# Performance work log

Measured on AMD Instinct MI355X. Metric: run time of the kernel, lower is better.

## Reference

```python
import jax, jax.numpy as jnp
import numpy as np

SR = 16000
N_TAPS = 10
MIN_F = 50.0
MAX_F = 2000.0


def setup_inputs() -> dict:
    key = jax.random.key(0)
    k1, k2 = jax.random.split(key)
    x = jax.random.normal(k1, (8, 1, 32000), dtype=jnp.float32)
    # raw f params as in the module: 3*(rand*2-1) in [-3, 3]
    f = 3.0 * (jax.random.uniform(k2, (128, 1), dtype=jnp.float32) * 2.0 - 1.0)
    a = jnp.full((128, 1), 0.9, dtype=jnp.float32)
    return {"x": x, "f": f, "a": a}


def _comb(x, f_raw, a):
    # scaling_function (min_freq/max_freq branch, no bins):
    # f = min_freq * (max_freq/min_freq) ** sigmoid(f_raw)
    fratio = MAX_F / MIN_F
    f = MIN_F * fratio ** jax.nn.sigmoid(f_raw)  # [O, I] fundamental freq in Hz

    B, I, T = x.shape
    O = f.shape[0]
    D = SR / f  # [O, I] fractional delay in samples (one period)
    n = jnp.arange(T, dtype=x.dtype)
    ci = jnp.arange(I)[None, :, None]  # channel index for gather, [1, I, 1]

    acc = jnp.zeros((B, O, T), dtype=x.dtype)
    # y[b,o,t] = sum_i sum_{k=0}^{n_taps-1} a[o,i]^k * lerp(x[b,i, t - k*D[o,i]])
    for k in range(N_TAPS):
        pos = n[None, None, :] - k * D[:, :, None]  # [O, I, T] fractional read positions
        i0 = jnp.floor(pos)
        frac = (pos - i0).astype(x.dtype)
        valid = (i0 >= 0).astype(x.dtype)  # causal: zero before signal start
        i0i = jnp.clip(i0.astype(jnp.int32), 0, T - 1)
        i1i = jnp.clip(i0i + 1, 0, T - 1)
        x0 = x[:, ci, i0i]  # [B, O, I, T]
        x1 = x[:, ci, i1i]  # [B, O, I, T]
        tap = (x0 * (1.0 - frac) + x1 * frac) * valid
        acc = acc + jnp.sum((a ** k)[None, :, :, None] * tap, axis=2)
    return acc


def reference(x, f, a):
    # use_bias=False -> b = 0, gain g unused in forward
    return _comb(x, f, a)
```

## Files before the change

### kernel.cpp

```cpp
#include <hip/hip_runtime.h>
#include <math.h>

#define T_LEN 32000
#define B_N 8
#define O_N 128
#define NTAPS 10
#define TILE_T 1280
#define NT 5
#define PAD 2944
#define NSTAGE (TILE_T + PAD + 1)
#define NSTAGE_AL ((NSTAGE + 3) & ~3)
#define OCHUNK 8
#define TC 640

__global__ __launch_bounds__(128) void comb_params_kernel(
    const float* __restrict__ f, const float* __restrict__ a,
    float* __restrict__ tp) {
  int o = threadIdx.x;
  double fr = (double)f[o];
  double sig = 1.0 / (1.0 + exp(-fr));
  float ff = (float)(50.0 * pow(40.0, sig));
  float D = 16000.0f / ff;
  float av = a[o];
  for (int k = 0; k < NTAPS; ++k) {
    tp[o * 20 + k] = (float)k * D;
    tp[o * 20 + 10 + k] = (float)pow((double)av, (double)k);
  }
}

__device__ __forceinline__ void comb_body_fast(const float* __restrict__ tp,
                                               float* __restrict__ outp,
                                               const float* sx, int oc,
                                               int t0, int tid) {
  float tcf = (float)(t0 + TC);
  int cbase = PAD - t0 - TC;
  float xt[NT];
#pragma unroll
  for (int j = 0; j < NT; ++j) xt[j] = sx[PAD + tid + 256 * j];
#pragma unroll 1
  for (int oi = 0; oi < OCHUNK; ++oi) {
    const float4* p4 = (const float4*)(tp + (oc + oi) * 20);
    float4 q0 = p4[0], q1 = p4[1], q2 = p4[2], q3 = p4[3], q4 = p4[4];
    float kD[NTAPS] = {q0.x, q0.y, q0.z, q0.w, q1.x, q1.y, q1.z, q1.w, q2.x, q2.y};
    float ak[NTAPS] = {q2.z, q2.w, q3.x, q3.y, q3.z, q3.w, q4.x, q4.y, q4.z, q4.w};
    float acc[NT];
#pragma unroll
    for (int j = 0; j < NT; ++j) acc[j] = xt[j];
#pragma unroll
    for (int k = 1; k < NTAPS; ++k) {
      float pc = tcf - kD[k];
      float fc = __builtin_amdgcn_fractf(pc);
      int sb = (int)(pc - fc) + cbase + tid;
      float w1 = ak[k] * fc;
      float w0 = ak[k] - w1;
#pragma unroll
      for (int j = 0; j < NT; ++j) {
        int idx = sb + 256 * j;
        float x0 = sx[idx];
        float x1 = sx[idx + 1];
        acc[j] = fmaf(w0, x0, fmaf(w1, x1, acc[j]));
      }
    }
#pragma unroll
    for (int j = 0; j < NT; ++j)
      outp[(size_t)oi * T_LEN + 256 * j] = acc[j];
  }
}

__device__ __forceinline__ void comb_body_edge(const float* __restrict__ tp,
                                               float* __restrict__ outp,
                                               const float* sx, int oc,
                                               const float* tf, int base_g) {
#pragma unroll 1
  for (int oi = 0; oi < OCHUNK; ++oi) {
    const float4* p4 = (const float4*)(tp + (oc + oi) * 20);
    float4 q0 = p4[0], q1 = p4[1], q2 = p4[2], q3 = p4[3], q4 = p4[4];
    float kD[NTAPS] = {q0.x, q0.y, q0.z, q0.w, q1.x, q1.y, q1.z, q1.w, q2.x, q2.y};
    float ak[NTAPS] = {q2.z, q2.w, q3.x, q3.y, q3.z, q3.w, q4.x, q4.y, q4.z, q4.w};
    float acc[NT];
#pragma unroll
    for (int j = 0; j < NT; ++j) acc[j] = 0.0f;
#pragma unroll
    for (int k = 0; k < NTAPS; ++k) {
#pragma unroll
      for (int j = 0; j < NT; ++j) {
        float pos = tf[j] - kD[k];
        float frac = __builtin_amdgcn_fractf(pos);
        int idx = (int)pos - base_g;
        float x0 = sx[idx];
        float x1 = sx[idx + 1];
        float tap = fmaf(frac, x1 - x0, x0);
        tap = (pos >= 0.0f) ? tap : 0.0f;
        acc[j] = fmaf(ak[k], tap, acc[j]);
      }
    }
#pragma unroll
    for (int j = 0; j < NT; ++j)
      outp[(size_t)oi * T_LEN + 256 * j] = acc[j];
  }
}

__global__ __launch_bounds__(256) void comb_main_kernel(
    const float* __restrict__ x, const float* __restrict__ tp,
    float* __restrict__ out) {
  __shared__ float sx[NSTAGE_AL];
  int bx = blockIdx.x;
  int t0 = bx * TILE_T;
  int b = blockIdx.y;
  int oc = blockIdx.z * OCHUNK;
  const float* __restrict__ xrow = x + b * T_LEN;
  int base_g = t0 - PAD;
  int tid = threadIdx.x;

  if (bx >= 3 && bx <= 23) {
    float4* s4 = (float4*)sx;
    const float4* g4 = (const float4*)(xrow + base_g);
#pragma unroll 1
    for (int j = tid; j < NSTAGE_AL / 4; j += 256) s4[j] = g4[j];
  } else {
#pragma unroll 1
    for (int j = tid; j < NSTAGE_AL; j += 256) {
      int g = base_g + j;
      float v = 0.0f;
      if (g >= 0) v = xrow[g < T_LEN - 1 ? g : T_LEN - 1];
      sx[j] = v;
    }
  }
  __syncthreads();

  float* outp = out + ((size_t)b * O_N + oc) * T_LEN + t0 + tid;

  if (bx >= 3) {
    comb_body_fast(tp, outp, sx, oc, t0, tid);
  } else {
    float tf[NT];
#pragma unroll
    for (int j = 0; j < NT; ++j) tf[j] = (float)(t0 + tid + 256 * j);
    comb_body_edge(tp, outp, sx, oc, tf, base_g);
  }
}

extern "C" void kernel_launch(void* const* d_in, const int* in_sizes, int n_in,
                              void* d_out, int out_size, void* d_ws,
                              size_t ws_size, hipStream_t stream) {
  const float* x = (const float*)d_in[0];
  const float* f = (const float*)d_in[1];
  const float* a = (const float*)d_in[2];
  float* out = (float*)d_out;
  float* tp = (float*)d_ws;

  comb_params_kernel<<<1, 128, 0, stream>>>(f, a, tp);

  dim3 grid(T_LEN / TILE_T, B_N, O_N / OCHUNK);
  comb_main_kernel<<<grid, 256, 0, stream>>>(x, tp, out);
}
```

Measured before the change: 174.0 us.

## Stage input as overlapping float2 pairs and give each thread contiguous outputs

The shared-memory stage now holds (x[i], x[i+1]) pairs as float2, so each lerp reads both neighbours in one 64-bit LDS load. Each thread now computes 5 consecutive output samples instead of samples strided by 256, so three float2 loads per tap cover all five outputs. This cuts LDS instruction count per tap, but doubles LDS footprint, makes global stores strided across lanes (5-float stride per thread), and risks LDS bank conflicts from the 5-element thread stride.

```diff
diff --git a/kernel.cpp b/kernel.cpp
--- a/kernel.cpp
+++ b/kernel.cpp
@@ -6,7 +6,6 @@
 #define O_N 128
 #define NTAPS 10
 #define TILE_T 1280
-#define NT 5
 #define PAD 2944
 #define NSTAGE (TILE_T + PAD + 1)
 #define NSTAGE_AL ((NSTAGE + 3) & ~3)
@@ -28,82 +27,82 @@
   }
 }
 
+#define LOAD_PARAMS                                                        \
+  const float4* p4 = (const float4*)(tp + (oc + oi) * 20);                 \
+  float4 q0 = p4[0], q1 = p4[1], q2 = p4[2], q3 = p4[3], q4 = p4[4];       \
+  float kD[NTAPS] = {q0.x, q0.y, q0.z, q0.w, q1.x,                         \
+                     q1.y, q1.z, q1.w, q2.x, q2.y};                        \
+  float ak[NTAPS] = {q2.z, q2.w, q3.x, q3.y, q3.z,                         \
+                     q3.w, q4.x, q4.y, q4.z, q4.w};
+
 __device__ __forceinline__ void comb_body_fast(const float* __restrict__ tp,
                                                float* __restrict__ outp,
-                                               const float* sx, int oc,
+                                               const float2* sx2, int oc,
                                                int t0, int tid) {
   float tcf = (float)(t0 + TC);
-  int cbase = PAD - t0 - TC;
-  float xt[NT];
-#pragma unroll
-  for (int j = 0; j < NT; ++j) xt[j] = sx[PAD + tid + 256 * j];
+  int cbase = PAD - t0 - TC + 5 * tid;
+  int b0 = PAD + 5 * tid;
+  float2 A0 = sx2[b0], B0 = sx2[b0 + 2], C0 = sx2[b0 + 4];
 #pragma unroll 1
   for (int oi = 0; oi < OCHUNK; ++oi) {
-    const float4* p4 = (const float4*)(tp + (oc + oi) * 20);
-    float4 q0 = p4[0], q1 = p4[1], q2 = p4[2], q3 = p4[3], q4 = p4[4];
-    float kD[NTAPS] = {q0.x, q0.y, q0.z, q0.w, q1.x, q1.y, q1.z, q1.w, q2.x, q2.y};
-    float ak[NTAPS] = {q2.z, q2.w, q3.x, q3.y, q3.z, q3.w, q4.x, q4.y, q4.z, q4.w};
-    float acc[NT];
-#pragma unroll
-    for (int j = 0; j < NT; ++j) acc[j] = xt[j];
+    LOAD_PARAMS
+    float acc[5] = {A0.x, A0.y, B0.x, B0.y, C0.x};
 #pragma unroll
     for (int k = 1; k < NTAPS; ++k) {
       float pc = tcf - kD[k];
       float fc = __builtin_amdgcn_fractf(pc);
-      int sb = (int)(pc - fc) + cbase + tid;
+      int sb = (int)(pc - fc) + cbase;
       float w1 = ak[k] * fc;
       float w0 = ak[k] - w1;
-#pragma unroll
-      for (int j = 0; j < NT; ++j) {
-        int idx = sb + 256 * j;
-        float x0 = sx[idx];
-        float x1 = sx[idx + 1];
-        acc[j] = fmaf(w0, x0, fmaf(w1, x1, acc[j]));
-      }
+      float2 A = sx2[sb];
+      float2 B = sx2[sb + 2];
+      float2 C = sx2[sb + 4];
+      acc[0] = fmaf(w0, A.x, fmaf(w1, A.y, acc[0]));
+      acc[1] = fmaf(w0, A.y, fmaf(w1, B.x, acc[1]));
+      acc[2] = fmaf(w0, B.x, fmaf(w1, B.y, acc[2]));
+      acc[3] = fmaf(w0, B.y, fmaf(w1, C.x, acc[3]));
+      acc[4] = fmaf(w0, C.x, fmaf(w1, C.y, acc[4]));
     }
 #pragma unroll
-    for (int j = 0; j < NT; ++j)
-      outp[(size_t)oi * T_LEN + 256 * j] = acc[j];
+    for (int u = 0; u < 5; ++u) outp[(size_t)oi * T_LEN + u] = acc[u];
   }
 }
 
 __device__ __forceinline__ void comb_body_edge(const float* __restrict__ tp,
                                                float* __restrict__ outp,
-                                               const float* sx, int oc,
-                                               const float* tf, int base_g) {
+                                               const float2* sx2, int oc,
+                                               int t0, int tid, int base_g) {
+  float tf[5];
+#pragma unroll
+  for (int u = 0; u < 5; ++u) tf[u] = (float)(t0 + 5 * tid + u);
 #pragma unroll 1
   for (int oi = 0; oi < OCHUNK; ++oi) {
-    const float4* p4 = (const float4*)(tp + (oc + oi) * 20);
-    float4 q0 = p4[0], q1 = p4[1], q2 = p4[2], q3 = p4[3], q4 = p4[4];
-    float kD[NTAPS] = {q0.x, q0.y, q0.z, q0.w, q1.x, q1.y, q1.z, q1.w, q2.x, q2.y};
-    float ak[NTAPS] = {q2.z, q2.w, q3.x, q3.y, q3.z, q3.w, q4.x, q4.y, q4.z, q4.w};
-    float acc[NT];
+    LOAD_PARAMS
+    float acc[5];
 #pragma unroll
-    for (int j = 0; j < NT; ++j) acc[j] = 0.0f;
+    for (int u = 0; u < 5; ++u) acc[u] = 0.0f;
 #pragma unroll
     for (int k = 0; k < NTAPS; ++k) {
 #pragma unroll
-      for (int j = 0; j < NT; ++j) {
-        float pos = tf[j] - kD[k];
+      for (int u = 0; u < 5; ++u) {
+        float pos = tf[u] - kD[k];
         float frac = __builtin_amdgcn_fractf(pos);
         int idx = (int)pos - base_g;
-        float x0 = sx[idx];
-        float x1 = sx[idx + 1];
-        float tap = fmaf(frac, x1 - x0, x0);
+        float2 xv = sx2[idx];
+        float tap = fmaf(frac, xv.y - xv.x, xv.x);
         tap = (pos >= 0.0f) ? tap : 0.0f;
-        acc[j] = fmaf(ak[k], tap, acc[j]);
+        acc[u] = fmaf(ak[k], tap, acc[u]);
       }
     }
 #pragma unroll
-    for (int j = 0; j < NT; ++j)
-      outp[(size_t)oi * T_LEN + 256 * j] = acc[j];
+    for (int u = 0; u < 5; ++u) outp[(size_t)oi * T_LEN + u] = acc[u];
   }
 }
 
 __global__ __launch_bounds__(256) void comb_main_kernel(
     const float* __restrict__ x, const float* __restrict__ tp,
     float* __restrict__ out) {
-  __shared__ float sx[NSTAGE_AL];
+  __shared__ float2 sx2[NSTAGE_AL];
   int bx = blockIdx.x;
   int t0 = bx * TILE_T;
   int b = blockIdx.y;
@@ -113,30 +112,34 @@
   int tid = threadIdx.x;
 
   if (bx >= 3 && bx <= 23) {
-    float4* s4 = (float4*)sx;
     const float4* g4 = (const float4*)(xrow + base_g);
 #pragma unroll 1
-    for (int j = tid; j < NSTAGE_AL / 4; j += 256) s4[j] = g4[j];
+    for (int j = tid; j < NSTAGE_AL / 4; j += 256) {
+      float4 v = g4[j];
+      float nx = xrow[base_g + 4 * j + 4];
+      sx2[4 * j + 0] = make_float2(v.x, v.y);
+      sx2[4 * j + 1] = make_float2(v.y, v.z);
+      sx2[4 * j + 2] = make_float2(v.z, v.w);
+      sx2[4 * j + 3] = make_float2(v.w, nx);
+    }
   } else {
 #pragma unroll 1
     for (int j = tid; j < NSTAGE_AL; j += 256) {
       int g = base_g + j;
-      float v = 0.0f;
-      if (g >= 0) v = xrow[g < T_LEN - 1 ? g : T_LEN - 1];
-      sx[j] = v;
+      float v0 = 0.0f, v1 = 0.0f;
+      if (g >= 0) v0 = xrow[g < T_LEN - 1 ? g : T_LEN - 1];
+      if (g + 1 >= 0) v1 = xrow[g + 1 < T_LEN - 1 ? g + 1 : T_LEN - 1];
+      sx2[j] = make_float2(v0, v1);
     }
   }
   __syncthreads();
 
-  float* outp = out + ((size_t)b * O_N + oc) * T_LEN + t0 + tid;
+  float* outp = out + ((size_t)b * O_N + oc) * T_LEN + t0 + 5 * tid;
 
   if (bx >= 3) {
-    comb_body_fast(tp, outp, sx, oc, t0, tid);
+    comb_body_fast(tp, outp, sx2, oc, t0, tid);
   } else {
-    float tf[NT];
-#pragma unroll
-    for (int j = 0; j < NT; ++j) tf[j] = (float)(t0 + tid + 256 * j);
-    comb_body_edge(tp, outp, sx, oc, tf, base_g);
+    comb_body_edge(tp, outp, sx2, oc, t0, tid, base_g);
   }
 }
 
```

Result: faster. 169.5 us (-2.6%).
